# Kernel tuning notes

Hardware: AMD Instinct MI355X
Metric: run time of the kernel (lower is better)

## Reference

```python
import jax, jax.numpy as jnp
import numpy as np

T, B, I, H = 2048, 128, 10, 512  # timesteps, batch, input_size, hidden_size


def setup_inputs() -> dict:
    key = jax.random.key(0)
    ks = jax.random.split(key, 7)
    s = 1.0 / np.sqrt(H)  # torch LSTMCell default init scale
    return {
        "x": jax.random.normal(ks[0], (T, B, I), dtype=jnp.float32),
        "hx": jax.random.normal(ks[1], (B, H), dtype=jnp.float32) * 0.1,
        "cx": jax.random.normal(ks[2], (B, H), dtype=jnp.float32) * 0.1,
        "W_ih": jax.random.uniform(ks[3], (4 * H, I), jnp.float32, -s, s),
        "W_hh": jax.random.uniform(ks[4], (4 * H, H), jnp.float32, -s, s),
        "b_ih": jax.random.uniform(ks[5], (4 * H,), jnp.float32, -s, s),
        "b_hh": jax.random.uniform(ks[6], (4 * H,), jnp.float32, -s, s),
    }


def reference(x, hx, cx, W_ih, W_hh, b_ih, b_hh):
    # Standard LSTMCell recurrence (PyTorch gate order: i, f, g, o).
    bias = b_ih + b_hh  # [4H]

    def step(carry, xt):
        h, c = carry  # [B,H], [B,H]
        gates = xt @ W_ih.T + h @ W_hh.T + bias  # [B,4H]
        i, f, g, o = jnp.split(gates, 4, axis=-1)
        i = jax.nn.sigmoid(i)
        f = jax.nn.sigmoid(f)
        g = jnp.tanh(g)
        o = jax.nn.sigmoid(o)
        c = f * c + i * g
        h = o * jnp.tanh(c)
        return (h, c), None

    (h, c), _ = jax.lax.scan(step, (hx, cx), x)  # scan over T
    # Original returns (x, (hx, cx)) where x == final hx.
    return (h, (h, c))
```

## Files before the change

### kernel.cpp

```cpp
#include <hip/hip_runtime.h>
#include <hip/hip_fp16.h>

#define T_STEPS 2048
#define B_SZ 128
#define I_SZ 10
#define H_SZ 512

#define NGRP 8
#define GWG 8
#define NWG (NGRP * GWG)
#define BSLICE 16
#define WCOL 64
#define NTHR 512

typedef _Float16 f16x8 __attribute__((ext_vector_type(8)));
typedef float f32x4 __attribute__((ext_vector_type(4)));
typedef float f32x2 __attribute__((ext_vector_type(2)));
typedef unsigned u32x4 __attribute__((ext_vector_type(4)));

__global__ void clear_flags_kernel(unsigned* p) {
    if (threadIdx.x < NGRP * 16)
        __hip_atomic_store(p + threadIdx.x, 0u,
                           __ATOMIC_RELAXED, __HIP_MEMORY_SCOPE_AGENT);
}

__global__ __launch_bounds__(NTHR, 2) void lstm_persistent(
    const float* __restrict__ x,
    const float* __restrict__ hx,
    const float* __restrict__ cx,
    const float* __restrict__ W_ih,
    const float* __restrict__ W_hh,
    const float* __restrict__ b_ih,
    const float* __restrict__ b_hh,
    float* __restrict__ out,
    unsigned* flags,
    _Float16* hbuf)
{
    __shared__ _Float16 h_stage[BSLICE][520];
    __shared__ float lds_g[4 * WCOL][17];

    const int wg   = blockIdx.x;
    const int g    = wg >> 3;
    const int wgin = wg & 7;
    const int tid  = threadIdx.x;
    const int wid  = tid >> 6;
    const int lane = tid & 63;
    const int fr_col = lane & 15;
    const int fr_kg  = lane >> 4;

    int gcL[2], wr[2];
    #pragma unroll
    for (int f = 0; f < 2; ++f) {
        gcL[f] = wid * 32 + f * 16 + fr_col;
        wr[f]  = (gcL[f] >> 6) * H_SZ + wgin * WCOL + (gcL[f] & 63);
    }

    f16x8 wf[2][16];
    #pragma unroll
    for (int f = 0; f < 2; ++f)
        #pragma unroll
        for (int c = 0; c < 16; ++c) {
            const float* p = W_hh + (size_t)wr[f] * H_SZ + c * 32 + fr_kg * 8;
            f16x8 w;
            #pragma unroll
            for (int e = 0; e < 8; ++e) w[e] = (_Float16)p[e];
            wf[f][c] = w;
        }

    float wih[2][I_SZ], bias[2];
    #pragma unroll
    for (int f = 0; f < 2; ++f) {
        #pragma unroll
        for (int i = 0; i < I_SZ; ++i) wih[f][i] = W_ih[wr[f] * I_SZ + i];
        bias[f] = b_ih[wr[f]] + b_hh[wr[f]];
    }

    const int orow  = tid >> 5;
    const int ocol  = wgin * WCOL + 2 * (tid & 31);
    const int gbrow = g * BSLICE + orow;

    float c0 = cx[gbrow * H_SZ + ocol];
    float c1 = cx[gbrow * H_SZ + ocol + 1];
    float h0 = hx[gbrow * H_SZ + ocol];
    float h1 = hx[gbrow * H_SZ + ocol + 1];

    const int srow  = tid & 15;
    const int scolb = tid >> 4;

    {
        _Float16* hb0 = hbuf + (size_t)g * (BSLICE * H_SZ);
        union { _Float16 hp[2]; unsigned u; } pk;
        pk.hp[0] = (_Float16)h0; pk.hp[1] = (_Float16)h1;
        __hip_atomic_store((unsigned*)(hb0 + orow * H_SZ + ocol), pk.u,
                           __ATOMIC_RELAXED, __HIP_MEMORY_SCOPE_AGENT);
    }
    asm volatile("s_waitcnt vmcnt(0)" ::: "memory");
    __syncthreads();
    if (tid == 0)
        __hip_atomic_store(flags + g * 16 + wgin, 1u,
                           __ATOMIC_RELAXED, __HIP_MEMORY_SCOPE_AGENT);

    #pragma unroll 1
    for (int t = 0; t < T_STEPS; ++t) {
        f32x4 acc[2];
        #pragma unroll
        for (int r = 0; r < 4; ++r) {
            const int grow = g * BSLICE + fr_kg * 4 + r;
            const f32x2* xp = (const f32x2*)(x + ((size_t)t * B_SZ + grow) * I_SZ);
            const f32x2 a0 = xp[0], a1 = xp[1], a2 = xp[2], a3 = xp[3], a4 = xp[4];
            #pragma unroll
            for (int f = 0; f < 2; ++f) {
                float s = bias[f];
                s += a0.x*wih[f][0] + a0.y*wih[f][1] + a1.x*wih[f][2] + a1.y*wih[f][3]
                   + a2.x*wih[f][4] + a2.y*wih[f][5] + a3.x*wih[f][6] + a3.y*wih[f][7]
                   + a4.x*wih[f][8] + a4.y*wih[f][9];
                acc[f][r] = s;
            }
        }

        if (wid == 0) {
            const unsigned tgt = (unsigned)(t + 1);
            const unsigned* fp = flags + g * 16 + (lane & 7);
            for (;;) {
                unsigned fv = __hip_atomic_load(fp, __ATOMIC_RELAXED,
                                                __HIP_MEMORY_SCOPE_AGENT);
                if (__all(fv >= tgt)) break;
                __builtin_amdgcn_s_sleep(2);
            }
        }
        __syncthreads();

        {
            const _Float16* hb = hbuf + ((size_t)(t & 1) * NGRP + g) * (BSLICE * H_SZ);
            const char* sp = (const char*)hb + srow * 1024 + scolb * 32;
            u32x4 qa, qb;
            asm volatile("global_load_dwordx4 %0, %2, off sc0 sc1\n\t"
                         "global_load_dwordx4 %1, %2, off offset:16 sc0 sc1\n\t"
                         "s_waitcnt vmcnt(0)"
                         : "=&v"(qa), "=&v"(qb) : "v"(sp) : "memory");
            *(u32x4*)&h_stage[srow][scolb * 16]     = qa;
            *(u32x4*)&h_stage[srow][scolb * 16 + 8] = qb;
        }
        __syncthreads();

        #pragma unroll
        for (int c = 0; c < 16; ++c) {
            const f16x8 a = *(const f16x8*)&h_stage[fr_col][c * 32 + fr_kg * 8];
            acc[0] = __builtin_amdgcn_mfma_f32_16x16x32_f16(a, wf[0][c], acc[0], 0, 0, 0);
            acc[1] = __builtin_amdgcn_mfma_f32_16x16x32_f16(a, wf[1][c], acc[1], 0, 0, 0);
        }

        #pragma unroll
        for (int f = 0; f < 2; ++f)
            #pragma unroll
            for (int r = 0; r < 4; ++r)
                lds_g[gcL[f]][fr_kg * 4 + r] = acc[f][r];
        __syncthreads();

        {
            const int cl = 2 * (tid & 31);
            const float i0 = lds_g[0 * WCOL + cl][orow],     f0 = lds_g[1 * WCOL + cl][orow];
            const float g0 = lds_g[2 * WCOL + cl][orow],     o0 = lds_g[3 * WCOL + cl][orow];
            const float i1 = lds_g[0 * WCOL + cl + 1][orow], f1 = lds_g[1 * WCOL + cl + 1][orow];
            const float g1 = lds_g[2 * WCOL + cl + 1][orow], o1 = lds_g[3 * WCOL + cl + 1][orow];

            const float ig0 = 1.f / (1.f + __expf(-i0));
            const float fg0 = 1.f / (1.f + __expf(-f0));
            const float eg0 = __expf(-2.f * g0);
            const float tg0 = (1.f - eg0) / (1.f + eg0);
            const float og0 = 1.f / (1.f + __expf(-o0));
            const float ig1 = 1.f / (1.f + __expf(-i1));
            const float fg1 = 1.f / (1.f + __expf(-f1));
            const float eg1 = __expf(-2.f * g1);
            const float tg1 = (1.f - eg1) / (1.f + eg1);
            const float og1 = 1.f / (1.f + __expf(-o1));

            c0 = fg0 * c0 + ig0 * tg0;
            c1 = fg1 * c1 + ig1 * tg1;
            const float e0 = __expf(-2.f * c0), e1 = __expf(-2.f * c1);
            h0 = og0 * (1.f - e0) / (1.f + e0);
            h1 = og1 * (1.f - e1) / (1.f + e1);

            if (t < T_STEPS - 1) {
                _Float16* hbn = hbuf + ((size_t)((t + 1) & 1) * NGRP + g)
                                        * (BSLICE * H_SZ);
                union { _Float16 hp[2]; unsigned u; } pk;
                pk.hp[0] = (_Float16)h0; pk.hp[1] = (_Float16)h1;
                __hip_atomic_store((unsigned*)(hbn + orow * H_SZ + ocol), pk.u,
                                   __ATOMIC_RELAXED, __HIP_MEMORY_SCOPE_AGENT);
            }
        }

        asm volatile("s_waitcnt vmcnt(0)" ::: "memory");
        __syncthreads();
        if (tid == 0 && t < T_STEPS - 1)
            __hip_atomic_store(flags + g * 16 + wgin, (unsigned)(t + 2),
                               __ATOMIC_RELAXED, __HIP_MEMORY_SCOPE_AGENT);
    }

    out[gbrow * H_SZ + ocol]                       = h0;
    out[gbrow * H_SZ + ocol + 1]                   = h1;
    out[B_SZ * H_SZ + gbrow * H_SZ + ocol]         = h0;
    out[B_SZ * H_SZ + gbrow * H_SZ + ocol + 1]     = h1;
    out[2 * B_SZ * H_SZ + gbrow * H_SZ + ocol]     = c0;
    out[2 * B_SZ * H_SZ + gbrow * H_SZ + ocol + 1] = c1;
}

extern "C" void kernel_launch(void* const* d_in, const int* in_sizes, int n_in,
                              void* d_out, int out_size, void* d_ws, size_t ws_size,
                              hipStream_t stream) {
    const float* x    = (const float*)d_in[0];
    const float* hx   = (const float*)d_in[1];
    const float* cx   = (const float*)d_in[2];
    const float* W_ih = (const float*)d_in[3];
    const float* W_hh = (const float*)d_in[4];
    const float* b_ih = (const float*)d_in[5];
    const float* b_hh = (const float*)d_in[6];
    float* out = (float*)d_out;

    char* ws = (char*)d_ws;
    unsigned* flags = (unsigned*)ws;
    _Float16* hbuf  = (_Float16*)(ws + 1024);

    clear_flags_kernel<<<1, 256, 0, stream>>>(flags);
    lstm_persistent<<<NWG, NTHR, 0, stream>>>(x, hx, cx, W_ih, W_hh, b_ih, b_hh,
                                              out, flags, hbuf);
}
```

Baseline: 7.780 ms.

## Replace per-workgroup flags with step-tagged hidden-state words for inline synchronization

Each fp16 hidden-state pair is now stored as a 64-bit word whose upper half carries the timestep tag. Consumers poll the data itself until every tag is current. This removes the separate flag array, the store-drain wait, the barrier and the flag store after each step, and the single-wave flag spin before the data load. In exchange, the hidden-state buffer traffic doubles and every wave polls global memory. Correctness rests on each 64-bit relaxed atomic store being seen as a whole, which keeps the tag and its data consistent.

```diff
diff --git a/kernel.cpp b/kernel.cpp
--- a/kernel.cpp
+++ b/kernel.cpp
@@ -17,10 +17,13 @@
 typedef float f32x4 __attribute__((ext_vector_type(4)));
 typedef float f32x2 __attribute__((ext_vector_type(2)));
 typedef unsigned u32x4 __attribute__((ext_vector_type(4)));
-
-__global__ void clear_flags_kernel(unsigned* p) {
-    if (threadIdx.x < NGRP * 16)
-        __hip_atomic_store(p + threadIdx.x, 0u,
+typedef unsigned long long u64t;
+
+__global__ void clear_hbuf_kernel(u64t* p) {
+    const int i = blockIdx.x * 256 + threadIdx.x;
+    #pragma unroll
+    for (int k = 0; k < 4; ++k)
+        __hip_atomic_store(p + i + k * 16384, 0ull,
                            __ATOMIC_RELAXED, __HIP_MEMORY_SCOPE_AGENT);
 }
 
@@ -33,8 +36,7 @@
     const float* __restrict__ b_ih,
     const float* __restrict__ b_hh,
     float* __restrict__ out,
-    unsigned* flags,
-    _Float16* hbuf)
+    u64t* hbuf)
 {
     __shared__ _Float16 h_stage[BSLICE][520];
     __shared__ float lds_g[4 * WCOL][17];
@@ -78,6 +80,7 @@
     const int orow  = tid >> 5;
     const int ocol  = wgin * WCOL + 2 * (tid & 31);
     const int gbrow = g * BSLICE + orow;
+    const size_t my_q = (size_t)orow * 256 + (ocol >> 1);
 
     float c0 = cx[gbrow * H_SZ + ocol];
     float c1 = cx[gbrow * H_SZ + ocol + 1];
@@ -85,20 +88,15 @@
     float h1 = hx[gbrow * H_SZ + ocol + 1];
 
     const int srow  = tid & 15;
-    const int scolb = tid >> 4;
+    const int schk  = tid >> 4;
 
     {
-        _Float16* hb0 = hbuf + (size_t)g * (BSLICE * H_SZ);
+        u64t* hb0 = hbuf + (size_t)g * (BSLICE * 256);
         union { _Float16 hp[2]; unsigned u; } pk;
         pk.hp[0] = (_Float16)h0; pk.hp[1] = (_Float16)h1;
-        __hip_atomic_store((unsigned*)(hb0 + orow * H_SZ + ocol), pk.u,
+        __hip_atomic_store(hb0 + my_q, ((u64t)1u << 32) | pk.u,
                            __ATOMIC_RELAXED, __HIP_MEMORY_SCOPE_AGENT);
     }
-    asm volatile("s_waitcnt vmcnt(0)" ::: "memory");
-    __syncthreads();
-    if (tid == 0)
-        __hip_atomic_store(flags + g * 16 + wgin, 1u,
-                           __ATOMIC_RELAXED, __HIP_MEMORY_SCOPE_AGENT);
 
     #pragma unroll 1
     for (int t = 0; t < T_STEPS; ++t) {
@@ -118,28 +116,34 @@
             }
         }
 
-        if (wid == 0) {
+        {
+            const u64t* hb = hbuf + ((size_t)(t & 1) * NGRP + g) * (BSLICE * 256);
+            const char* sp = (const char*)(hb + (size_t)srow * 256 + schk * 8);
             const unsigned tgt = (unsigned)(t + 1);
-            const unsigned* fp = flags + g * 16 + (lane & 7);
+            bool done = false;
             for (;;) {
-                unsigned fv = __hip_atomic_load(fp, __ATOMIC_RELAXED,
-                                                __HIP_MEMORY_SCOPE_AGENT);
-                if (__all(fv >= tgt)) break;
-                __builtin_amdgcn_s_sleep(2);
+                if (!done) {
+                    u32x4 qa, qb, qc, qd;
+                    asm volatile(
+                        "global_load_dwordx4 %0, %4, off sc0 sc1\n\t"
+                        "global_load_dwordx4 %1, %4, off offset:16 sc0 sc1\n\t"
+                        "global_load_dwordx4 %2, %4, off offset:32 sc0 sc1\n\t"
+                        "global_load_dwordx4 %3, %4, off offset:48 sc0 sc1\n\t"
+                        "s_waitcnt vmcnt(0)"
+                        : "=&v"(qa), "=&v"(qb), "=&v"(qc), "=&v"(qd)
+                        : "v"(sp) : "memory");
+                    if (qa.y >= tgt && qa.w >= tgt && qb.y >= tgt && qb.w >= tgt &&
+                        qc.y >= tgt && qc.w >= tgt && qd.y >= tgt && qd.w >= tgt) {
+                        const u32x4 p0 = {qa.x, qa.z, qb.x, qb.z};
+                        const u32x4 p1 = {qc.x, qc.z, qd.x, qd.z};
+                        *(u32x4*)&h_stage[srow][schk * 16]     = p0;
+                        *(u32x4*)&h_stage[srow][schk * 16 + 8] = p1;
+                        done = true;
+                    }
+                }
+                if (__all(done)) break;
+                __builtin_amdgcn_s_sleep(1);
             }
-        }
-        __syncthreads();
-
-        {
-            const _Float16* hb = hbuf + ((size_t)(t & 1) * NGRP + g) * (BSLICE * H_SZ);
-            const char* sp = (const char*)hb + srow * 1024 + scolb * 32;
-            u32x4 qa, qb;
-            asm volatile("global_load_dwordx4 %0, %2, off sc0 sc1\n\t"
-                         "global_load_dwordx4 %1, %2, off offset:16 sc0 sc1\n\t"
-                         "s_waitcnt vmcnt(0)"
-                         : "=&v"(qa), "=&v"(qb) : "v"(sp) : "memory");
-            *(u32x4*)&h_stage[srow][scolb * 16]     = qa;
-            *(u32x4*)&h_stage[srow][scolb * 16 + 8] = qb;
         }
         __syncthreads();
 
@@ -182,20 +186,14 @@
             h1 = og1 * (1.f - e1) / (1.f + e1);
 
             if (t < T_STEPS - 1) {
-                _Float16* hbn = hbuf + ((size_t)((t + 1) & 1) * NGRP + g)
-                                        * (BSLICE * H_SZ);
+                u64t* hbn = hbuf + ((size_t)((t + 1) & 1) * NGRP + g) * (BSLICE * 256);
                 union { _Float16 hp[2]; unsigned u; } pk;
                 pk.hp[0] = (_Float16)h0; pk.hp[1] = (_Float16)h1;
-                __hip_atomic_store((unsigned*)(hbn + orow * H_SZ + ocol), pk.u,
+                __hip_atomic_store(hbn + my_q,
+                                   ((u64t)(unsigned)(t + 2) << 32) | pk.u,
                                    __ATOMIC_RELAXED, __HIP_MEMORY_SCOPE_AGENT);
             }
         }
-
-        asm volatile("s_waitcnt vmcnt(0)" ::: "memory");
-        __syncthreads();
-        if (tid == 0 && t < T_STEPS - 1)
-            __hip_atomic_store(flags + g * 16 + wgin, (unsigned)(t + 2),
-                               __ATOMIC_RELAXED, __HIP_MEMORY_SCOPE_AGENT);
     }
 
     out[gbrow * H_SZ + ocol]                       = h0;
@@ -218,11 +216,9 @@
     const float* b_hh = (const float*)d_in[6];
     float* out = (float*)d_out;
 
-    char* ws = (char*)d_ws;
-    unsigned* flags = (unsigned*)ws;
-    _Float16* hbuf  = (_Float16*)(ws + 1024);
-
-    clear_flags_kernel<<<1, 256, 0, stream>>>(flags);
+    u64t* hbuf = (u64t*)d_ws;
+
+    clear_hbuf_kernel<<<64, 256, 0, stream>>>(hbuf);
     lstm_persistent<<<NWG, NTHR, 0, stream>>>(x, hx, cx, W_ih, W_hh, b_ih, b_hh,
-                                              out, flags, hbuf);
+                                              out, hbuf);
 }
```

Result: slower. 8.334 ms (+7.1%).

## Use per-wave completion flags and drop block barriers around the grid handshake

Applied to the files above, without the earlier changes.

Each wave now publishes its own progress flag right after storing its slice of h. Every wave polls all 64 flags of its batch group directly, which removes the two __syncthreads that surrounded the flag wait and the flag publish. The h staging load is remapped so each wave fetches whole rows, and the poll sleep is shortened. In exchange there is eight times more flag polling traffic per workgroup, and the flag region and clear kernel grow to match.

```diff
diff --git a/kernel.cpp b/kernel.cpp
--- a/kernel.cpp
+++ b/kernel.cpp
@@ -19,9 +19,9 @@
 typedef unsigned u32x4 __attribute__((ext_vector_type(4)));
 
 __global__ void clear_flags_kernel(unsigned* p) {
-    if (threadIdx.x < NGRP * 16)
-        __hip_atomic_store(p + threadIdx.x, 0u,
-                           __ATOMIC_RELAXED, __HIP_MEMORY_SCOPE_AGENT);
+    const int i = blockIdx.x * 256 + threadIdx.x;
+    if (i < NGRP * 64)
+        __hip_atomic_store(p + i, 0u, __ATOMIC_RELAXED, __HIP_MEMORY_SCOPE_AGENT);
 }
 
 __global__ __launch_bounds__(NTHR, 2) void lstm_persistent(
@@ -84,8 +84,7 @@
     float h0 = hx[gbrow * H_SZ + ocol];
     float h1 = hx[gbrow * H_SZ + ocol + 1];
 
-    const int srow  = tid & 15;
-    const int scolb = tid >> 4;
+    unsigned* myflag = flags + g * 64 + wgin * 8 + wid;
 
     {
         _Float16* hb0 = hbuf + (size_t)g * (BSLICE * H_SZ);
@@ -95,10 +94,8 @@
                            __ATOMIC_RELAXED, __HIP_MEMORY_SCOPE_AGENT);
     }
     asm volatile("s_waitcnt vmcnt(0)" ::: "memory");
-    __syncthreads();
-    if (tid == 0)
-        __hip_atomic_store(flags + g * 16 + wgin, 1u,
-                           __ATOMIC_RELAXED, __HIP_MEMORY_SCOPE_AGENT);
+    if (lane == 0)
+        __hip_atomic_store(myflag, 1u, __ATOMIC_RELAXED, __HIP_MEMORY_SCOPE_AGENT);
 
     #pragma unroll 1
     for (int t = 0; t < T_STEPS; ++t) {
@@ -118,28 +115,28 @@
             }
         }
 
-        if (wid == 0) {
+        {
             const unsigned tgt = (unsigned)(t + 1);
-            const unsigned* fp = flags + g * 16 + (lane & 7);
+            const unsigned* fp = flags + g * 64 + lane;
             for (;;) {
                 unsigned fv = __hip_atomic_load(fp, __ATOMIC_RELAXED,
                                                 __HIP_MEMORY_SCOPE_AGENT);
                 if (__all(fv >= tgt)) break;
-                __builtin_amdgcn_s_sleep(2);
+                __builtin_amdgcn_s_sleep(1);
             }
         }
-        __syncthreads();
 
         {
             const _Float16* hb = hbuf + ((size_t)(t & 1) * NGRP + g) * (BSLICE * H_SZ);
-            const char* sp = (const char*)hb + srow * 1024 + scolb * 32;
+            const char* sp = (const char*)hb + wid * 2048 + lane * 16;
             u32x4 qa, qb;
-            asm volatile("global_load_dwordx4 %0, %2, off sc0 sc1\n\t"
-                         "global_load_dwordx4 %1, %2, off offset:16 sc0 sc1\n\t"
-                         "s_waitcnt vmcnt(0)"
-                         : "=&v"(qa), "=&v"(qb) : "v"(sp) : "memory");
-            *(u32x4*)&h_stage[srow][scolb * 16]     = qa;
-            *(u32x4*)&h_stage[srow][scolb * 16 + 8] = qb;
+            asm volatile(
+                "global_load_dwordx4 %0, %2, off sc0 sc1\n\t"
+                "global_load_dwordx4 %1, %2, off offset:1024 sc0 sc1\n\t"
+                "s_waitcnt vmcnt(0)"
+                : "=&v"(qa), "=&v"(qb) : "v"(sp) : "memory");
+            *(u32x4*)&h_stage[2 * wid][lane * 8]     = qa;
+            *(u32x4*)&h_stage[2 * wid + 1][lane * 8] = qb;
         }
         __syncthreads();
 
@@ -188,14 +185,12 @@
                 pk.hp[0] = (_Float16)h0; pk.hp[1] = (_Float16)h1;
                 __hip_atomic_store((unsigned*)(hbn + orow * H_SZ + ocol), pk.u,
                                    __ATOMIC_RELAXED, __HIP_MEMORY_SCOPE_AGENT);
+                asm volatile("s_waitcnt vmcnt(0)" ::: "memory");
+                if (lane == 0)
+                    __hip_atomic_store(myflag, (unsigned)(t + 2),
+                                       __ATOMIC_RELAXED, __HIP_MEMORY_SCOPE_AGENT);
             }
         }
-
-        asm volatile("s_waitcnt vmcnt(0)" ::: "memory");
-        __syncthreads();
-        if (tid == 0 && t < T_STEPS - 1)
-            __hip_atomic_store(flags + g * 16 + wgin, (unsigned)(t + 2),
-                               __ATOMIC_RELAXED, __HIP_MEMORY_SCOPE_AGENT);
     }
 
     out[gbrow * H_SZ + ocol]                       = h0;
@@ -220,9 +215,9 @@
 
     char* ws = (char*)d_ws;
     unsigned* flags = (unsigned*)ws;
-    _Float16* hbuf  = (_Float16*)(ws + 1024);
-
-    clear_flags_kernel<<<1, 256, 0, stream>>>(flags);
+    _Float16* hbuf  = (_Float16*)(ws + 4096);
+
+    clear_flags_kernel<<<2, 256, 0, stream>>>(flags);
     lstm_persistent<<<NWG, NTHR, 0, stream>>>(x, hx, cx, W_ih, W_hh, b_ih, b_hh,
                                               out, flags, hbuf);
 }
```

Result: slower. 10.17 ms (+30.8%).
